# Optimization experiments

Hardware: AMD Instinct MI355X
Metric: run time of the kernel (lower is better)

The kernel has to match this reference:

```python
import jax, jax.numpy as jnp
import numpy as np

# Mamba2 dims (defaults: expand=2, d_state=128, d_conv=4, ngroups=1)
D_MODEL = 1024
HEADDIM = 64
D_STATE = 128
D_CONV = 4
D_INNER = 2 * D_MODEL            # 2048
NHEADS = D_INNER // HEADDIM      # 32
CONV_DIM = D_INNER + 2 * D_STATE # 2304
D_IN_PROJ = 2 * D_INNER + 2 * D_STATE + NHEADS  # 4384
EPS = 1e-5


def setup_inputs() -> dict:
    key = jax.random.key(0)
    ks = jax.random.split(key, 12)
    B, L = 4, 2048
    inp = {}
    inp['query'] = jax.random.normal(ks[0], (B, L, D_MODEL), jnp.float32)
    inp['key'] = jax.random.normal(ks[1], (B, L, D_MODEL), jnp.float32)
    inp['value'] = jax.random.normal(ks[2], (B, L, D_MODEL), jnp.float32)
    # parameters (Mamba2-style init)
    inp['in_proj_w'] = jax.random.normal(ks[3], (D_IN_PROJ, D_MODEL), jnp.float32) * (D_MODEL ** -0.5)
    inp['conv_w'] = jax.random.normal(ks[4], (CONV_DIM, D_CONV), jnp.float32) * (D_CONV ** -0.5)
    inp['conv_b'] = jnp.zeros((CONV_DIM,), jnp.float32)
    # dt init: softplus^{-1}(dt) with dt ~ U[1e-3, 1e-1]
    dt = jnp.exp(jax.random.uniform(ks[5], (NHEADS,)) * (np.log(0.1) - np.log(1e-3)) + np.log(1e-3))
    inp['dt_bias'] = dt + jnp.log(-jnp.expm1(-dt))
    # A ~ U[1, 16], A_log = log(A)
    inp['A_log'] = jnp.log(jax.random.uniform(ks[6], (NHEADS,), minval=1.0, maxval=16.0))
    inp['D'] = jnp.ones((NHEADS,), jnp.float32)
    inp['norm_w'] = jnp.ones((D_INNER,), jnp.float32)
    inp['out_proj_w'] = jax.random.normal(ks[7], (D_MODEL, D_INNER), jnp.float32) * (D_INNER ** -0.5)
    return inp


def _mamba2_forward(u, in_proj_w, conv_w, conv_b, dt_bias, A_log, D, norm_w, out_proj_w):
    b, l, _ = u.shape
    zxbcdt = jnp.einsum('bld,ed->ble', u, in_proj_w)  # (b,l,D_IN_PROJ)
    z = zxbcdt[..., :D_INNER]
    xBC = zxbcdt[..., D_INNER:D_INNER + CONV_DIM]
    dt = jax.nn.softplus(zxbcdt[..., -NHEADS:] + dt_bias)  # (b,l,h)
    # depthwise causal conv1d over time, kernel D_CONV, + silu
    xBC_pad = jnp.pad(xBC, ((0, 0), (D_CONV - 1, 0), (0, 0)))
    conv = conv_b
    for k in range(D_CONV):
        conv = conv + xBC_pad[:, k:k + l, :] * conv_w[:, k]
    xBC = jax.nn.silu(conv)
    x = xBC[..., :D_INNER].reshape(b, l, NHEADS, HEADDIM)   # (b,l,h,p)
    Bm = xBC[..., D_INNER:D_INNER + D_STATE]                # (b,l,n) ngroups=1
    Cm = xBC[..., D_INNER + D_STATE:]                       # (b,l,n)
    A = -jnp.exp(A_log)                                      # (h,)
    dA = jnp.exp(dt * A)                                     # (b,l,h)

    def step(h, inputs):
        dA_t, dt_t, x_t, B_t, C_t = inputs  # (b,h),(b,h),(b,h,p),(b,n),(b,n)
        h = h * dA_t[:, :, None, None] + (dt_t[:, :, None, None] * x_t[..., None]) * B_t[:, None, None, :]
        y = jnp.einsum('bhpn,bn->bhp', h, C_t)
        return h, y

    h0 = jnp.zeros((b, NHEADS, HEADDIM, D_STATE), u.dtype)
    xs = (dA.transpose(1, 0, 2), dt.transpose(1, 0, 2), x.transpose(1, 0, 2, 3),
          Bm.transpose(1, 0, 2), Cm.transpose(1, 0, 2))
    _, ys = jax.lax.scan(step, h0, xs)
    y = ys.transpose(1, 0, 2, 3) + x * D[None, None, :, None]  # (b,l,h,p)
    y = y.reshape(b, l, D_INNER)
    # RMSNormGated (norm_before_gate=False): norm(y * silu(z)) * w
    y = y * jax.nn.silu(z)
    y = y * jax.lax.rsqrt(jnp.mean(y * y, axis=-1, keepdims=True) + EPS) * norm_w
    return jnp.einsum('ble,de->bld', y, out_proj_w)


def reference(query, key, value, in_proj_w, conv_w, conv_b, dt_bias, A_log, D, norm_w, out_proj_w):
    # wrapper ignores key/value; returns mamba(query) (cache pass-through omitted)
    return _mamba2_forward(query, in_proj_w, conv_w, conv_b, dt_bias, A_log, D, norm_w, out_proj_w)
```

## Files before the change

kernel.cpp:

```cpp
#include <hip/hip_runtime.h>
#include <hip/hip_bf16.h>


typedef __attribute__((ext_vector_type(8))) short bf16x8;
typedef __attribute__((ext_vector_type(4))) float f32x4;

static constexpr int B_ = 4;
static constexpr int L_ = 2048;
static constexpr int NROWS = B_ * L_;
static constexpr int DMODEL = 1024;
static constexpr int DINNER = 2048;
static constexpr int NH = 32;
static constexpr int DSTATE = 128;
static constexpr int CONVDIM = DINNER + 2 * DSTATE;
static constexpr int DINPROJ = 2 * DINNER + 2 * DSTATE + NH;
static constexpr int Q_ = 64;
static constexpr int NCHUNK = L_ / Q_;

__device__ __forceinline__ unsigned pk_bf16(float a, float b) {
  unsigned ua = __builtin_bit_cast(unsigned, a);
  unsigned ub = __builtin_bit_cast(unsigned, b);
  ua = (ua + 0x7FFFu + ((ua >> 16) & 1u)) >> 16;
  ub = (ub + 0x7FFFu + ((ub >> 16) & 1u)) >> 16;
  return (ua & 0xFFFFu) | (ub << 16);
}
__device__ __forceinline__ unsigned short bf16_of(float a) {
  unsigned ua = __builtin_bit_cast(unsigned, a);
  return (unsigned short)((ua + 0x7FFFu + ((ua >> 16) & 1u)) >> 16);
}
__device__ __forceinline__ float f_of_bf16(unsigned short s) {
  return __builtin_bit_cast(float, (unsigned)s << 16);
}
__device__ __forceinline__ unsigned short* state_slot(unsigned short* lo,
                                                      unsigned short* hi,
                                                      int bh, int c) {
  int i = bh * NCHUNK + c;
  return (i < 2048) ? lo + (size_t)i * 8192 : hi + (size_t)(i - 2048) * 8192;
}

__global__ __launch_bounds__(256) void cast4_kernel(const float* __restrict__ in,
                                                    unsigned short* __restrict__ out) {
  int i = blockIdx.x * 256 + threadIdx.x;
  float4 v = ((const float4*)in)[i];
  ((uint2*)out)[i] = make_uint2(pk_bf16(v.x, v.y), pk_bf16(v.z, v.w));
}

#define WAITVM(N) asm volatile("s_waitcnt vmcnt(" #N ")" ::: "memory")

template <int BM, bool C_BF16>
__global__ __launch_bounds__(512, 1) void gemm256_kernel(
    const unsigned short* __restrict__ A, const unsigned short* __restrict__ Bw,
    void* __restrict__ Cp, int M, int N, int K, int lda, int ldb, int ldc) {
  (void)M;
  constexpr int MI = BM / 32;
  constexpr int TOTROWS = BM + 256;
  constexpr int RPW = TOTROWS / 8;
  constexpr int NLD = RPW / 16;
  __shared__ unsigned short sAB[4 * TOTROWS * 32];
  const int tid = threadIdx.x;
  const int w = tid >> 6;
  const int lane = tid & 63;
  const int quad = lane >> 4;
  const int r15 = lane & 15;

  const int NT = gridDim.x;
  const int orig = blockIdx.y * NT + blockIdx.x;
  const int xcd = orig & 7;
  const int loc = orig >> 3;
  const int mPerX = gridDim.y >> 3;
  const int m0 = (xcd * mPerX + (loc % mPerX)) * BM;
  const int n0 = (loc / mPerX) * 256;

  const int wm = w >> 2;
  const int wn = w & 3;

  const unsigned short* gsrc[NLD];
  int lofs[NLD];
#pragma unroll
  for (int ld = 0; ld < NLD; ++ld) {
    int r16 = w * RPW + ld * 16;
    int row = r16 + (lane >> 2);
    int ca = ((lane & 3) ^ ((row >> 1) & 3)) * 8;
    gsrc[ld] = (r16 < BM) ? A + (size_t)(m0 + row) * lda + ca
                          : Bw + (size_t)(n0 + row - BM) * ldb + ca;
    lofs[ld] = r16 * 32;
  }
  const int nslice = K >> 5;

  f32x4 acc[MI][4];
#pragma unroll
  for (int i = 0; i < MI; ++i)
#pragma unroll
    for (int j = 0; j < 4; ++j) acc[i][j] = f32x4{0.f, 0.f, 0.f, 0.f};

  auto ldsAB = (__attribute__((address_space(3))) unsigned short*)sAB;

  auto stage = [&](int ks) {
    const int so = (ks & 3) * (TOTROWS * 32);
#pragma unroll
    for (int ld = 0; ld < NLD; ++ld)
      __builtin_amdgcn_global_load_lds(
          (const __attribute__((address_space(1))) void*)(gsrc[ld] + (size_t)ks * 32),
          (__attribute__((address_space(3))) void*)(ldsAB + so + lofs[ld]), 16, 0, 0);
  };

  const int kx = (quad ^ ((r15 >> 1) & 3)) * 8;

  bf16x8 af[MI], bf[4];

#define READF(S)                                                                \
  {                                                                             \
    const int so_ = ((S) & 3) * (TOTROWS * 32);                                 \
    _Pragma("unroll") for (int i = 0; i < MI; ++i)                              \
        af[i] = *(const bf16x8*)&sAB[so_ + (wm * (BM / 2) + i * 16 + r15) * 32 + kx]; \
    _Pragma("unroll") for (int j = 0; j < 4; ++j)                               \
        bf[j] = *(const bf16x8*)&sAB[so_ + (BM + wn * 64 + j * 16 + r15) * 32 + kx];  \
  }
#define MFMAC()                                                                 \
  _Pragma("unroll") for (int i = 0; i < MI; ++i)                                \
      _Pragma("unroll") for (int j = 0; j < 4; ++j)                             \
          acc[i][j] = __builtin_amdgcn_mfma_f32_16x16x32_bf16(af[i], bf[j],     \
                                                              acc[i][j], 0, 0, 0);

#define WVM_STEADY do { if constexpr (NLD == 4) WAITVM(8); else WAITVM(6); } while (0)
#define WVM_TAIL1  do { if constexpr (NLD == 4) WAITVM(4); else WAITVM(3); } while (0)

  stage(0);
  stage(1);
  stage(2);
  WVM_STEADY;
  __builtin_amdgcn_s_barrier();
  __builtin_amdgcn_sched_barrier(0);

#define GITER(STAGE_STMT, WVM_STMT)                                             \
  {                                                                             \
    READF(s);                                                                   \
    STAGE_STMT;                                                                 \
    __builtin_amdgcn_s_barrier();                                               \
    asm volatile("s_waitcnt lgkmcnt(0)" ::: "memory");                          \
    __builtin_amdgcn_sched_barrier(0);                                          \
    __builtin_amdgcn_s_setprio(1);                                              \
    MFMAC();                                                                    \
    __builtin_amdgcn_s_setprio(0);                                              \
    WVM_STMT;                                                                   \
    __builtin_amdgcn_s_barrier();                                               \
    __builtin_amdgcn_sched_barrier(0);                                          \
  }

  int s = 0;
  for (; s < nslice - 3; ++s) GITER(stage(s + 3), WVM_STEADY);
  GITER((void)0, WVM_TAIL1);
  ++s;
  GITER((void)0, WAITVM(0));
  ++s;
  GITER((void)0, WAITVM(0));
#undef GITER
#undef WVM_STEADY
#undef WVM_TAIL1
#undef MFMAC
#undef READF

  const int rq = quad * 4;
#pragma unroll
  for (int i = 0; i < MI; ++i) {
#pragma unroll
    for (int j = 0; j < 4; ++j) {
      int gcol = n0 + wn * 64 + j * 16 + r15;
      if (gcol < N) {
#pragma unroll
        for (int r = 0; r < 4; ++r) {
          size_t grow = (size_t)(m0 + wm * (BM / 2) + i * 16 + rq + r);
          if constexpr (C_BF16)
            ((unsigned short*)Cp)[grow * (size_t)ldc + gcol] = bf16_of(acc[i][j][r]);
          else
            ((float*)Cp)[grow * (size_t)ldc + gcol] = acc[i][j][r];
        }
      }
    }
  }
}

__global__ __launch_bounds__(256) void conv_kernel(const unsigned short* __restrict__ zx,
                                                   const float* __restrict__ conv_w,
                                                   const float* __restrict__ conv_b,
                                                   unsigned short* __restrict__ xbc) {
  int c = blockIdx.x * 256 + threadIdx.x;
  int row = blockIdx.y;
  int l = row & (L_ - 1);
  float acc = conv_b[c];
#pragma unroll
  for (int k = 0; k < 4; ++k) {
    int ll = l + k - 3;
    if (ll >= 0)
      acc = fmaf(f_of_bf16(zx[(size_t)(row + k - 3) * DINPROJ + DINNER + c]),
                 conv_w[c * 4 + k], acc);
  }
  acc = acc / (1.f + __expf(-acc));
  xbc[(size_t)row * CONVDIM + c] = bf16_of(acc);
}

__global__ __launch_bounds__(256) void dt_kernel(const unsigned short* __restrict__ zx,
                                                 const float* __restrict__ dt_bias,
                                                 float* __restrict__ dtv) {
  int i = blockIdx.x * 256 + threadIdx.x;
  int hh = i & (NH - 1);
  int row = i >> 5;
  float x = f_of_bf16(zx[(size_t)row * DINPROJ + DINNER + CONVDIM + hh]) + dt_bias[hh];
  dtv[i] = (x > 20.f) ? x : log1pf(__expf(x));
}

__global__ __launch_bounds__(256) void ssd_passA(unsigned short* __restrict__ xbc,
                                                 const float* __restrict__ dtv,
                                                 const float* __restrict__ A_log,
                                                 const float* __restrict__ Dvec,
                                                 unsigned short* __restrict__ st_lo,
                                                 unsigned short* __restrict__ st_hi) {
  const int bid = blockIdx.x;
  const int h = bid & 31;
  const int c = (bid >> 5) & 31;
  const int b = bid >> 10;
  const int bh = b * 32 + h;
  const int tid = threadIdx.x;
  const int w = tid >> 6;
  const int lane = tid & 63;
  const int quad = lane >> 4;
  const int c15 = lane & 15;

  __shared__ unsigned short sXt[64 * 72];
  __shared__ unsigned short sBq[64 * 136];
  __shared__ unsigned short sCB[128 * 72];
  __shared__ float sdt[64], scs[64], sg[64];

  const float A = -__expf(A_log[h]);
  const float Dh = Dvec[h];
  const int r0 = b * L_ + c * Q_;

  if (w == 0) {
    float v = dtv[(size_t)(r0 + lane) * NH + h];
    sdt[lane] = v;
    float s = v;
#pragma unroll
    for (int off = 1; off < 64; off <<= 1) {
      float t = __shfl_up(s, off, 64);
      if (lane >= off) s += t;
    }
    scs[lane] = s;
    float T = __shfl(s, 63, 64);
    sg[lane] = __expf(A * (T - s)) * v;
  }
  for (int e = tid; e < 512; e += 256) {
    int t = e & 63, pb = e >> 6;
    uint4 v = *(const uint4*)&xbc[(size_t)(r0 + t) * CONVDIM + h * 64 + pb * 8];
    const unsigned short* sv = (const unsigned short*)&v;
#pragma unroll
    for (int j = 0; j < 8; ++j) sXt[(pb * 8 + j) * 72 + t] = sv[j];
  }
  for (int e = tid; e < 1024; e += 256) {
    int s = e >> 4, ch = e & 15;
    size_t roff = (size_t)(r0 + s) * CONVDIM + DINNER;
    *(uint4*)&sBq[s * 136 + ch * 8] = *(const uint4*)&xbc[roff + ch * 8];
    *(uint4*)&sCB[s * 136 + ch * 8] = *(const uint4*)&xbc[roff + DSTATE + ch * 8];
  }
  __syncthreads();

  const int wt = w >> 1, wx = w & 1;
  f32x4 sacc[2][2];
#pragma unroll
  for (int i = 0; i < 2; ++i)
#pragma unroll
    for (int j = 0; j < 2; ++j) sacc[i][j] = f32x4{0.f, 0.f, 0.f, 0.f};
#pragma unroll
  for (int kk = 0; kk < 4; ++kk) {
    int k8 = quad * 8 + kk * 32;
    bf16x8 a0 = *(const bf16x8*)&sCB[(wt * 32 + c15) * 136 + k8];
    bf16x8 a1 = *(const bf16x8*)&sCB[(wt * 32 + 16 + c15) * 136 + k8];
    bf16x8 b0 = *(const bf16x8*)&sBq[(wx * 32 + c15) * 136 + k8];
    bf16x8 b1 = *(const bf16x8*)&sBq[(wx * 32 + 16 + c15) * 136 + k8];
    sacc[0][0] = __builtin_amdgcn_mfma_f32_16x16x32_bf16(a0, b0, sacc[0][0], 0, 0, 0);
    sacc[0][1] = __builtin_amdgcn_mfma_f32_16x16x32_bf16(a0, b1, sacc[0][1], 0, 0, 0);
    sacc[1][0] = __builtin_amdgcn_mfma_f32_16x16x32_bf16(a1, b0, sacc[1][0], 0, 0, 0);
    sacc[1][1] = __builtin_amdgcn_mfma_f32_16x16x32_bf16(a1, b1, sacc[1][1], 0, 0, 0);
  }
  __syncthreads();

#pragma unroll
  for (int i = 0; i < 2; ++i)
#pragma unroll
    for (int j = 0; j < 2; ++j) {
      int scol = wx * 32 + j * 16 + c15;
      float css = scs[scol], dts = sdt[scol];
#pragma unroll
      for (int r = 0; r < 4; ++r) {
        int trow = wt * 32 + i * 16 + quad * 4 + r;
        float v = (scol <= trow) ? sacc[i][j][r] * __expf(A * (scs[trow] - css)) * dts : 0.f;
        sBq[trow * 72 + scol] = bf16_of(v);
      }
    }
  for (int e = tid; e < 1024; e += 256) {
    int s = e & 63, nb = e >> 6;
    uint4 v = *(const uint4*)&xbc[(size_t)(r0 + s) * CONVDIM + DINNER + nb * 8];
    float g = sg[s];
    const unsigned short* sv = (const unsigned short*)&v;
#pragma unroll
    for (int j = 0; j < 8; ++j)
      sCB[(nb * 8 + j) * 72 + s] = bf16_of(f_of_bf16(sv[j]) * g);
  }
  __syncthreads();

  f32x4 yacc[2][2];
#pragma unroll
  for (int i = 0; i < 2; ++i)
#pragma unroll
    for (int j = 0; j < 2; ++j) yacc[i][j] = f32x4{0.f, 0.f, 0.f, 0.f};
#pragma unroll
  for (int kk = 0; kk < 2; ++kk) {
    int k8 = quad * 8 + kk * 32;
    bf16x8 a0 = *(const bf16x8*)&sBq[(wt * 32 + c15) * 72 + k8];
    bf16x8 a1 = *(const bf16x8*)&sBq[(wt * 32 + 16 + c15) * 72 + k8];
    bf16x8 b0 = *(const bf16x8*)&sXt[(wx * 32 + c15) * 72 + k8];
    bf16x8 b1 = *(const bf16x8*)&sXt[(wx * 32 + 16 + c15) * 72 + k8];
    yacc[0][0] = __builtin_amdgcn_mfma_f32_16x16x32_bf16(a0, b0, yacc[0][0], 0, 0, 0);
    yacc[0][1] = __builtin_amdgcn_mfma_f32_16x16x32_bf16(a0, b1, yacc[0][1], 0, 0, 0);
    yacc[1][0] = __builtin_amdgcn_mfma_f32_16x16x32_bf16(a1, b0, yacc[1][0], 0, 0, 0);
    yacc[1][1] = __builtin_amdgcn_mfma_f32_16x16x32_bf16(a1, b1, yacc[1][1], 0, 0, 0);
  }
#pragma unroll
  for (int i = 0; i < 2; ++i)
#pragma unroll
    for (int j = 0; j < 2; ++j) {
      int p = wx * 32 + j * 16 + c15;
#pragma unroll
      for (int r = 0; r < 4; ++r) {
        int t = wt * 32 + i * 16 + quad * 4 + r;
        float xv = f_of_bf16(sXt[p * 72 + t]);
        xbc[(size_t)(r0 + t) * CONVDIM + h * 64 + p] = bf16_of(yacc[i][j][r] + Dh * xv);
      }
    }

  f32x4 hacc[2][4];
#pragma unroll
  for (int i = 0; i < 2; ++i)
#pragma unroll
    for (int j = 0; j < 4; ++j) hacc[i][j] = f32x4{0.f, 0.f, 0.f, 0.f};
  const int wp = w >> 1, wn = w & 1;
#pragma unroll
  for (int kk = 0; kk < 2; ++kk) {
    int k8 = quad * 8 + kk * 32;
    bf16x8 a0 = *(const bf16x8*)&sXt[(wp * 32 + c15) * 72 + k8];
    bf16x8 a1 = *(const bf16x8*)&sXt[(wp * 32 + 16 + c15) * 72 + k8];
    bf16x8 bfr[4];
#pragma unroll
    for (int j = 0; j < 4; ++j)
      bfr[j] = *(const bf16x8*)&sCB[(wn * 64 + j * 16 + c15) * 72 + k8];
#pragma unroll
    for (int j = 0; j < 4; ++j) {
      hacc[0][j] = __builtin_amdgcn_mfma_f32_16x16x32_bf16(a0, bfr[j], hacc[0][j], 0, 0, 0);
      hacc[1][j] = __builtin_amdgcn_mfma_f32_16x16x32_bf16(a1, bfr[j], hacc[1][j], 0, 0, 0);
    }
  }
  unsigned short* slot = state_slot(st_lo, st_hi, bh, c);
#pragma unroll
  for (int i = 0; i < 2; ++i)
#pragma unroll
    for (int j = 0; j < 4; ++j)
#pragma unroll
      for (int r = 0; r < 4; ++r) {
        int p = wp * 32 + i * 16 + quad * 4 + r;
        int n = wn * 64 + j * 16 + c15;
        slot[p * 128 + n] = bf16_of(hacc[i][j][r]);
      }
}

__global__ __launch_bounds__(256) void ssd_passB(const float* __restrict__ dtv,
                                                 const float* __restrict__ A_log,
                                                 unsigned short* __restrict__ st_lo,
                                                 unsigned short* __restrict__ st_hi) {
  const int bh = blockIdx.x >> 1;
  const int ph = blockIdx.x & 1;
  const int h = bh & 31;
  const int b = bh >> 5;
  const int tid = threadIdx.x;
  __shared__ float sd[NCHUNK];
  const float A = -__expf(A_log[h]);
  if (tid < NCHUNK) {
    float s = 0.f;
    const float* dp = dtv + (size_t)(b * L_ + tid * Q_) * NH + h;
    for (int i = 0; i < Q_; ++i) s += dp[(size_t)i * NH];
    sd[tid] = __expf(A * s);
  }
  __syncthreads();
  float hreg[16];
#pragma unroll
  for (int k = 0; k < 16; ++k) hreg[k] = 0.f;
  const size_t eoff = (size_t)ph * 4096 + (size_t)tid * 16;
  for (int c = 0; c < NCHUNK; ++c) {
    unsigned short* sp = state_slot(st_lo, st_hi, bh, c) + eoff;
    uint4 t0 = ((const uint4*)sp)[0];
    uint4 t1 = ((const uint4*)sp)[1];
    unsigned o[8];
#pragma unroll
    for (int k = 0; k < 8; ++k) o[k] = pk_bf16(hreg[2 * k], hreg[2 * k + 1]);
    ((uint4*)sp)[0] = make_uint4(o[0], o[1], o[2], o[3]);
    ((uint4*)sp)[1] = make_uint4(o[4], o[5], o[6], o[7]);
    float d = sd[c];
    const unsigned short* tv0 = (const unsigned short*)&t0;
    const unsigned short* tv1 = (const unsigned short*)&t1;
#pragma unroll
    for (int k = 0; k < 8; ++k) hreg[k] = d * hreg[k] + f_of_bf16(tv0[k]);
#pragma unroll
    for (int k = 0; k < 8; ++k) hreg[8 + k] = d * hreg[8 + k] + f_of_bf16(tv1[k]);
  }
}

__global__ __launch_bounds__(256) void ssd_passC(unsigned short* __restrict__ xbc,
                                                 const float* __restrict__ dtv,
                                                 const float* __restrict__ A_log,
                                                 const unsigned short* __restrict__ st_lo,
                                                 const unsigned short* __restrict__ st_hi) {
  const int bid = blockIdx.x;
  const int h = bid & 31;
  const int c = (bid >> 5) & 31;
  const int b = bid >> 10;
  const int bh = b * 32 + h;
  const int tid = threadIdx.x;
  const int w = tid >> 6;
  const int lane = tid & 63;
  const int quad = lane >> 4;
  const int c15 = lane & 15;

  __shared__ unsigned short sC[64 * 136];
  __shared__ unsigned short sH[64 * 136];
  __shared__ float srt[64];

  const float A = -__expf(A_log[h]);
  const int r0 = b * L_ + c * Q_;

  if (w == 0) {
    float v = dtv[(size_t)(r0 + lane) * NH + h];
    float s = v;
#pragma unroll
    for (int off = 1; off < 64; off <<= 1) {
      float t = __shfl_up(s, off, 64);
      if (lane >= off) s += t;
    }
    srt[lane] = __expf(A * s);
  }
  const unsigned short* slot =
      state_slot((unsigned short*)st_lo, (unsigned short*)st_hi, bh, c);
  for (int e = tid; e < 1024; e += 256) {
    int s = e >> 4, ch = e & 15;
    *(uint4*)&sC[s * 136 + ch * 8] =
        *(const uint4*)&xbc[(size_t)(r0 + s) * CONVDIM + DINNER + DSTATE + ch * 8];
    *(uint4*)&sH[s * 136 + ch * 8] = *(const uint4*)&slot[s * 128 + ch * 8];
  }
  __syncthreads();

  const int wt = w >> 1, wx = w & 1;
  f32x4 yacc[2][2];
#pragma unroll
  for (int i = 0; i < 2; ++i)
#pragma unroll
    for (int j = 0; j < 2; ++j) yacc[i][j] = f32x4{0.f, 0.f, 0.f, 0.f};
#pragma unroll
  for (int kk = 0; kk < 4; ++kk) {
    int k8 = quad * 8 + kk * 32;
    bf16x8 a0 = *(const bf16x8*)&sC[(wt * 32 + c15) * 136 + k8];
    bf16x8 a1 = *(const bf16x8*)&sC[(wt * 32 + 16 + c15) * 136 + k8];
    bf16x8 b0 = *(const bf16x8*)&sH[(wx * 32 + c15) * 136 + k8];
    bf16x8 b1 = *(const bf16x8*)&sH[(wx * 32 + 16 + c15) * 136 + k8];
    yacc[0][0] = __builtin_amdgcn_mfma_f32_16x16x32_bf16(a0, b0, yacc[0][0], 0, 0, 0);
    yacc[0][1] = __builtin_amdgcn_mfma_f32_16x16x32_bf16(a0, b1, yacc[0][1], 0, 0, 0);
    yacc[1][0] = __builtin_amdgcn_mfma_f32_16x16x32_bf16(a1, b0, yacc[1][0], 0, 0, 0);
    yacc[1][1] = __builtin_amdgcn_mfma_f32_16x16x32_bf16(a1, b1, yacc[1][1], 0, 0, 0);
  }
#pragma unroll
  for (int i = 0; i < 2; ++i)
#pragma unroll
    for (int j = 0; j < 2; ++j) {
      int p = wx * 32 + j * 16 + c15;
#pragma unroll
      for (int r = 0; r < 4; ++r) {
        int t = wt * 32 + i * 16 + quad * 4 + r;
        size_t ga = (size_t)(r0 + t) * CONVDIM + h * 64 + p;
        float v = yacc[i][j][r] * srt[t] + f_of_bf16(xbc[ga]);
        xbc[ga] = bf16_of(v);
      }
    }
}

__global__ __launch_bounds__(256) void norm_kernel(const unsigned short* __restrict__ y_in,
                                                   unsigned short* __restrict__ zxb,
                                                   const float* __restrict__ norm_w) {
  const int row = blockIdx.x;
  const int tid = threadIdx.x;
  float v[8];
  float ss = 0.f;
#pragma unroll
  for (int i = 0; i < 8; ++i) {
    int c = tid + i * 256;
    float yv = f_of_bf16(y_in[(size_t)row * CONVDIM + c]);
    float z = f_of_bf16(zxb[(size_t)row * DINPROJ + c]);
    yv *= z / (1.f + __expf(-z));
    v[i] = yv;
    ss = fmaf(yv, yv, ss);
  }
#pragma unroll
  for (int o = 32; o > 0; o >>= 1) ss += __shfl_down(ss, o, 64);
  __shared__ float sred[4];
  if ((tid & 63) == 0) sred[tid >> 6] = ss;
  __syncthreads();
  float tot = (sred[0] + sred[1]) + (sred[2] + sred[3]);
  float r = rsqrtf(tot * (1.f / (float)DINNER) + 1e-5f);
#pragma unroll
  for (int i = 0; i < 8; ++i) {
    int c = tid + i * 256;
    zxb[(size_t)row * DINPROJ + c] = bf16_of(v[i] * r * norm_w[c]);
  }
}

extern "C" void kernel_launch(void* const* d_in, const int* in_sizes, int n_in,
                              void* d_out, int out_size, void* d_ws, size_t ws_size,
                              hipStream_t stream) {
  (void)in_sizes; (void)n_in; (void)out_size;
  const float* u          = (const float*)d_in[0];
  const float* in_proj_w  = (const float*)d_in[3];
  const float* conv_w     = (const float*)d_in[4];
  const float* conv_b     = (const float*)d_in[5];
  const float* dt_bias    = (const float*)d_in[6];
  const float* A_log      = (const float*)d_in[7];
  const float* Dvec       = (const float*)d_in[8];
  const float* norm_w     = (const float*)d_in[9];
  const float* out_proj_w = (const float*)d_in[10];
  float* out = (float*)d_out;

  constexpr size_t SZ_ZX   = (size_t)NROWS * DINPROJ * 2;
  constexpr size_t SZ_XBC  = (size_t)NROWS * CONVDIM * 2;
  constexpr size_t SZ_DT   = (size_t)NROWS * NH * 4;
  constexpr size_t SZ_SHR  = 33554432;
  constexpr size_t SZ_WOUT = (size_t)DMODEL * DINNER * 2;
  constexpr size_t NEED = SZ_ZX + SZ_XBC + SZ_DT + SZ_SHR + SZ_WOUT;
  if (ws_size < NEED) return;

  char* p = (char*)d_ws;
  unsigned short* zxb  = (unsigned short*)p; p += SZ_ZX;
  unsigned short* xbc  = (unsigned short*)p; p += SZ_XBC;
  float* dtv           = (float*)p;          p += SZ_DT;
  char* shared_reg     = p;                  p += SZ_SHR;
  unsigned short* wout_bf = (unsigned short*)p;

  unsigned short* u_bf   = (unsigned short*)shared_reg;
  unsigned short* win_bf = (unsigned short*)(shared_reg + 16777216);
  unsigned short* st_lo  = (unsigned short*)d_out;
  unsigned short* st_hi  = (unsigned short*)shared_reg;

  cast4_kernel<<<(NROWS * DMODEL) / 1024, 256, 0, stream>>>(u, u_bf);
  cast4_kernel<<<(DINPROJ * DMODEL) / 1024, 256, 0, stream>>>(in_proj_w, win_bf);
  cast4_kernel<<<(DMODEL * DINNER) / 1024, 256, 0, stream>>>(out_proj_w, wout_bf);

  gemm256_kernel<256, true><<<dim3(18, 32), 512, 0, stream>>>(
      u_bf, win_bf, zxb, NROWS, DINPROJ, DMODEL, DMODEL, DMODEL, DINPROJ);
  conv_kernel<<<dim3(9, NROWS), 256, 0, stream>>>(zxb, conv_w, conv_b, xbc);
  dt_kernel<<<(NROWS * NH) / 256, 256, 0, stream>>>(zxb, dt_bias, dtv);

  ssd_passA<<<B_ * NCHUNK * NH, 256, 0, stream>>>(xbc, dtv, A_log, Dvec, st_lo, st_hi);
  ssd_passB<<<B_ * NH * 2, 256, 0, stream>>>(dtv, A_log, st_lo, st_hi);
  ssd_passC<<<B_ * NCHUNK * NH, 256, 0, stream>>>(xbc, dtv, A_log, st_lo, st_hi);

  norm_kernel<<<NROWS, 256, 0, stream>>>(xbc, zxb, norm_w);
  gemm256_kernel<128, false><<<dim3(4, 64), 512, 0, stream>>>(
      zxb, wout_bf, out, NROWS, DMODEL, DINNER, DINPROJ, DINNER, DMODEL);
}
```

Before: 485.8 us.

## Add 8-wave ping-pong phased GEMM kernel for input projection

Introduces a new 256x256-tile bf16 GEMM that double-buffers K=64 slices in LDS through direct global-to-LDS loads. Each K step is split into four phases that interleave LDS fragment reads, async staging of the next tile, and MFMA quarters, separated by barriers and raised wave priority. The in_proj GEMM now uses this kernel. The goal is to hide global load latency behind MFMA work, at the cost of more barriers and higher register pressure from the 8x4 accumulators. Rows of B beyond N appear to be read past the weight's 4384 rows, relying on the workspace layout.

```diff
diff --git a/kernel.cpp b/kernel.cpp
--- a/kernel.cpp
+++ b/kernel.cpp
@@ -46,6 +46,155 @@
 }
 
 #define WAITVM(N) asm volatile("s_waitcnt vmcnt(" #N ")" ::: "memory")
+
+template <bool C_BF16>
+__global__ __launch_bounds__(512, 1) void gemm8p_kernel(
+    const unsigned short* __restrict__ A, const unsigned short* __restrict__ Bw,
+    void* __restrict__ Cp, int N, int K, int lda, int ldb, int ldc) {
+  __shared__ unsigned short sAB[2 * 4 * 128 * 64];
+  const int tid = threadIdx.x;
+  const int w = tid >> 6;
+  const int lane = tid & 63;
+  const int quad = lane >> 4;
+  const int r15 = lane & 15;
+  const int wm = w >> 2;
+  const int wn = w & 3;
+
+  const int NT = gridDim.x;
+  const int orig = blockIdx.y * NT + blockIdx.x;
+  const int xcd = orig & 7;
+  const int loc = orig >> 3;
+  const int mPerX = gridDim.y >> 3;
+  const int m0 = (xcd * mPerX + (loc % mPerX)) * 256;
+  const int n0 = (loc / mPerX) * 256;
+
+  const int srow = tid >> 3;
+  const int px = ((tid & 7) ^ (srow & 7)) * 8;
+  const unsigned short* gA = A + (size_t)(m0 + srow) * lda + px;
+  const unsigned short* gB = Bw + (size_t)(n0 + srow) * ldb + px;
+  auto ldsAB = (__attribute__((address_space(3))) unsigned short*)sAB;
+  const int dst = w * 512;
+
+  auto stageA = [&](int buf, int hi, int kt) {
+    const unsigned short* s0 = gA + (size_t)(hi * 128) * lda + (size_t)kt * 64;
+    int d = buf + (hi ? 3 : 0) * 8192 + dst;
+    __builtin_amdgcn_global_load_lds(
+        (const __attribute__((address_space(1))) void*)s0,
+        (__attribute__((address_space(3))) void*)(ldsAB + d), 16, 0, 0);
+    __builtin_amdgcn_global_load_lds(
+        (const __attribute__((address_space(1))) void*)(s0 + (size_t)64 * lda),
+        (__attribute__((address_space(3))) void*)(ldsAB + d + 4096), 16, 0, 0);
+  };
+  auto stageB = [&](int buf, int hi, int kt) {
+    const unsigned short* s0 = gB + (size_t)(hi * 128) * ldb + (size_t)kt * 64;
+    int d = buf + (hi ? 2 : 1) * 8192 + dst;
+    __builtin_amdgcn_global_load_lds(
+        (const __attribute__((address_space(1))) void*)s0,
+        (__attribute__((address_space(3))) void*)(ldsAB + d), 16, 0, 0);
+    __builtin_amdgcn_global_load_lds(
+        (const __attribute__((address_space(1))) void*)(s0 + (size_t)64 * ldb),
+        (__attribute__((address_space(3))) void*)(ldsAB + d + 4096), 16, 0, 0);
+  };
+
+  const int px0 = (quad ^ (r15 & 7)) * 8;
+  const int px1 = ((quad + 4) ^ (r15 & 7)) * 8;
+  const int aslot = (wm ? 3 : 0) * 8192;
+  const int bslot = ((wn >> 1) ? 2 : 1) * 8192;
+  const int arow0 = r15 * 64;
+  const int brow0 = ((wn & 1) * 64 + r15) * 64;
+
+  f32x4 acc[8][4];
+#pragma unroll
+  for (int i = 0; i < 8; ++i)
+#pragma unroll
+    for (int j = 0; j < 4; ++j) acc[i][j] = f32x4{0.f, 0.f, 0.f, 0.f};
+
+  bf16x8 af[4][2], bfr[2][2][2];
+
+#define READ_A(BUF, HI)                                                         \
+  _Pragma("unroll") for (int ii = 0; ii < 4; ++ii) {                            \
+    int ba = (BUF) + aslot + arow0 + (HI) * 4096 + ii * 1024;                   \
+    af[ii][0] = *(const bf16x8*)&sAB[ba + px0];                                 \
+    af[ii][1] = *(const bf16x8*)&sAB[ba + px1];                                 \
+  }
+#define READ_B(BUF, HJ)                                                         \
+  _Pragma("unroll") for (int jj = 0; jj < 2; ++jj) {                            \
+    int bb = (BUF) + bslot + brow0 + (HJ) * 2048 + jj * 1024;                   \
+    bfr[HJ][jj][0] = *(const bf16x8*)&sAB[bb + px0];                            \
+    bfr[HJ][jj][1] = *(const bf16x8*)&sAB[bb + px1];                            \
+  }
+#define MFMA_Q(HI, HJ)                                                          \
+  _Pragma("unroll") for (int ii = 0; ii < 4; ++ii)                              \
+    _Pragma("unroll") for (int jj = 0; jj < 2; ++jj) {                          \
+      acc[(HI) * 4 + ii][(HJ) * 2 + jj] = __builtin_amdgcn_mfma_f32_16x16x32_bf16( \
+          af[ii][0], bfr[HJ][jj][0], acc[(HI) * 4 + ii][(HJ) * 2 + jj], 0, 0, 0);  \
+      acc[(HI) * 4 + ii][(HJ) * 2 + jj] = __builtin_amdgcn_mfma_f32_16x16x32_bf16( \
+          af[ii][1], bfr[HJ][jj][1], acc[(HI) * 4 + ii][(HJ) * 2 + jj], 0, 0, 0);  \
+    }
+#define PHASE(READS, STAGES, MFMAQ, VMW)                                        \
+  {                                                                             \
+    READS;                                                                      \
+    STAGES;                                                                     \
+    __builtin_amdgcn_s_barrier();                                               \
+    asm volatile("s_waitcnt lgkmcnt(0)" ::: "memory");                          \
+    __builtin_amdgcn_sched_barrier(0);                                          \
+    __builtin_amdgcn_s_setprio(1);                                              \
+    MFMAQ;                                                                      \
+    __builtin_amdgcn_s_setprio(0);                                              \
+    VMW;                                                                        \
+    __builtin_amdgcn_s_barrier();                                               \
+    __builtin_amdgcn_sched_barrier(0);                                          \
+  }
+
+  const int nt = K >> 6;
+  stageA(0, 0, 0);
+  stageA(0, 1, 0);
+  stageB(0, 0, 0);
+  stageB(0, 1, 0);
+  WAITVM(0);
+  __builtin_amdgcn_s_barrier();
+  __builtin_amdgcn_sched_barrier(0);
+
+  for (int t = 0; t < nt; ++t) {
+    const int buf = (t & 1) * 32768;
+    const int nb = ((t + 1) & 1) * 32768;
+    const bool more = (t + 1 < nt);
+    const int k1 = t + 1;
+    PHASE(READ_A(buf, 0); READ_B(buf, 0),
+          if (more) stageA(nb, 0, k1),
+          MFMA_Q(0, 0), (void)0);
+    PHASE(READ_B(buf, 1),
+          if (more) stageA(nb, 1, k1),
+          MFMA_Q(0, 1), (void)0);
+    PHASE(READ_A(buf, 1),
+          if (more) { stageB(nb, 0, k1); stageB(nb, 1, k1); },
+          MFMA_Q(1, 1), (void)0);
+    PHASE((void)0, (void)0, MFMA_Q(1, 0), WAITVM(0));
+  }
+#undef PHASE
+#undef MFMA_Q
+#undef READ_B
+#undef READ_A
+
+  const int rq = quad * 4;
+#pragma unroll
+  for (int i = 0; i < 8; ++i) {
+#pragma unroll
+    for (int j = 0; j < 4; ++j) {
+      int gcol = n0 + wn * 64 + j * 16 + r15;
+      if (gcol < N) {
+#pragma unroll
+        for (int r = 0; r < 4; ++r) {
+          size_t grow = (size_t)(m0 + wm * 128 + i * 16 + rq + r);
+          if constexpr (C_BF16)
+            ((unsigned short*)Cp)[grow * (size_t)ldc + gcol] = bf16_of(acc[i][j][r]);
+          else
+            ((float*)Cp)[grow * (size_t)ldc + gcol] = acc[i][j][r];
+        }
+      }
+    }
+  }
+}
 
 template <int BM, bool C_BF16>
 __global__ __launch_bounds__(512, 1) void gemm256_kernel(
@@ -557,8 +706,8 @@
   cast4_kernel<<<(DINPROJ * DMODEL) / 1024, 256, 0, stream>>>(in_proj_w, win_bf);
   cast4_kernel<<<(DMODEL * DINNER) / 1024, 256, 0, stream>>>(out_proj_w, wout_bf);
 
-  gemm256_kernel<256, true><<<dim3(18, 32), 512, 0, stream>>>(
-      u_bf, win_bf, zxb, NROWS, DINPROJ, DMODEL, DMODEL, DMODEL, DINPROJ);
+  gemm8p_kernel<true><<<dim3(18, 32), 512, 0, stream>>>(
+      u_bf, win_bf, zxb, DINPROJ, DMODEL, DMODEL, DMODEL, DINPROJ);
   conv_kernel<<<dim3(9, NROWS), 256, 0, stream>>>(zxb, conv_w, conv_b, xbc);
   dt_kernel<<<(NROWS * NH) / 256, 256, 0, stream>>>(zxb, dt_bias, dtv);
 
```

New measurement: 489.9 us. About the same (+0.8%).
